# Performance work log

Hardware: AMD Instinct MI355X
Metric: run time of the kernel (lower is better)

## Reference

```python
import jax, jax.numpy as jnp
import numpy as np

B, S, D = 4, 2048, 1024
H = 16
DK = D // H  # 64, dim_k == dim_v
FF = 4096
EPS = 1e-5


def layer_norm(x, g, b):
    mu = jnp.mean(x, axis=-1, keepdims=True)
    var = jnp.mean(jnp.square(x - mu), axis=-1, keepdims=True)
    return (x - mu) * jax.lax.rsqrt(var + EPS) * g + b


def setup_inputs() -> dict:
    key = jax.random.key(0)
    ks = jax.random.split(key, 16)
    s = 0.02
    return {
        "src": jax.random.normal(ks[0], (B, S, D), jnp.float32),
        # per-head Q/K/V projections (stacked over heads)
        "wq": jax.random.normal(ks[1], (H, D, DK), jnp.float32) * s,
        "bq": jnp.zeros((H, DK), jnp.float32),
        "wk": jax.random.normal(ks[2], (H, D, DK), jnp.float32) * s,
        "bk": jnp.zeros((H, DK), jnp.float32),
        "wv": jax.random.normal(ks[3], (H, D, DK), jnp.float32) * s,
        "bv": jnp.zeros((H, DK), jnp.float32),
        # output projection: concat(H*DK) -> D
        "wo": jax.random.normal(ks[4], (H * DK, D), jnp.float32) * s,
        "bo": jnp.zeros((D,), jnp.float32),
        "ln1_g": jnp.ones((D,), jnp.float32),
        "ln1_b": jnp.zeros((D,), jnp.float32),
        # FFN
        "w1": jax.random.normal(ks[5], (D, FF), jnp.float32) * s,
        "b1": jnp.zeros((FF,), jnp.float32),
        "w2": jax.random.normal(ks[6], (FF, D), jnp.float32) * s,
        "b2": jnp.zeros((D,), jnp.float32),
        "ln2_g": jnp.ones((D,), jnp.float32),
        "ln2_b": jnp.zeros((D,), jnp.float32),
    }


def reference(src, wq, bq, wk, bk, wv, bv, wo, bo, ln1_g, ln1_b,
              w1, b1, w2, b2, ln2_g, ln2_b):
    # per-head projections: [B,S,D] x [H,D,K] -> [B,H,S,K]
    q = jnp.einsum('bsd,hdk->bhsk', src, wq) + bq[None, :, None, :]
    k = jnp.einsum('bsd,hdk->bhsk', src, wk) + bk[None, :, None, :]
    v = jnp.einsum('bsd,hdk->bhsk', src, wv) + bv[None, :, None, :]
    scale = 1.0 / jnp.sqrt(jnp.float32(DK))
    scores = jnp.einsum('bhsk,bhtk->bhst', q, k) * scale  # [B,H,S,S]
    attn = jax.nn.softmax(scores, axis=-1)
    o = jnp.einsum('bhst,bhtv->bhsv', attn, v)            # [B,H,S,DK]
    o = o.transpose(0, 2, 1, 3).reshape(B, S, H * DK)      # concat heads
    attn_out = o @ wo + bo
    x = layer_norm(src + attn_out, ln1_g, ln1_b)
    ff = jax.nn.relu(x @ w1 + b1) @ w2 + b2
    return layer_norm(x + ff, ln2_g, ln2_b)
```

## Files before the change

### kernel.cpp

```cpp
#include <hip/hip_runtime.h>

typedef __bf16 bf16;
typedef __bf16 bf16x8 __attribute__((ext_vector_type(8)));
typedef __bf16 bf16x4 __attribute__((ext_vector_type(4)));
typedef float  f32x4  __attribute__((ext_vector_type(4)));
typedef float  f32x16 __attribute__((ext_vector_type(16)));
typedef unsigned int u32;
typedef int i32x2 __attribute__((ext_vector_type(2)));

#define NB 4
#define NS 2048
#define ND 1024
#define NH 16
#define NDK 64
#define NFF 4096
#define NM (NB*NS)

#define QSCALE 0.18033688f

__device__ __forceinline__ void load_lds16(const void* g, void* l) {
  __builtin_amdgcn_global_load_lds(
      (const __attribute__((address_space(1))) void*)g,
      (__attribute__((address_space(3))) void*)l, 16, 0, 0);
}

__device__ __forceinline__ u32 pack2(float a, float b) {
  union { bf16 h[2]; u32 u; } z;
  z.h[0] = (bf16)a; z.h[1] = (bf16)b;
  return z.u;
}

__device__ __forceinline__ i32x2 pswap(u32 a, u32 b) {
#if __has_builtin(__builtin_amdgcn_permlane32_swap)
  return __builtin_amdgcn_permlane32_swap((int)a, (int)b, false, false);
#else
  u32 x = a, y = b;
  asm volatile("v_permlane32_swap_b32 %0, %1" : "+v"(x), "+v"(y));
  i32x2 r; r[0] = (int)x; r[1] = (int)y; return r;
#endif
}

__global__ __launch_bounds__(256)
void cvt_f32_bf16(const float* __restrict__ in, bf16* __restrict__ out, int n) {
  int i = (blockIdx.x * 256 + threadIdx.x) * 4;
  if (i < n) {
    float4 v = *(const float4*)&in[i];
    bf16x4 o;
    o[0] = (bf16)v.x; o[1] = (bf16)v.y; o[2] = (bf16)v.z; o[3] = (bf16)v.w;
    *(bf16x4*)&out[i] = o;
  }
}

__global__ __launch_bounds__(256)
void transpose_cvt(const float* __restrict__ in, bf16* __restrict__ out,
                   int R, int C, size_t in_bs, size_t out_bs) {
  __shared__ float t[32][33];
  int bx = blockIdx.x, by = blockIdx.y, bz = blockIdx.z;
  const float* ip = in + (size_t)bz * in_bs + (size_t)(bx * 32) * C + by * 32;
  bf16* op = out + (size_t)bz * out_bs + (size_t)(by * 32) * R + bx * 32;
  int x = threadIdx.x & 31, y = threadIdx.x >> 5;
#pragma unroll
  for (int yy = 0; yy < 32; yy += 8)
    t[y + yy][x] = ip[(size_t)(y + yy) * C + x];
  __syncthreads();
#pragma unroll
  for (int yy = 0; yy < 32; yy += 8)
    op[(size_t)(y + yy) * R + x] = (bf16)t[x][y + yy];
}

__global__ __launch_bounds__(256)
void transpose_v(const bf16* __restrict__ v, bf16* __restrict__ vT) {
  __shared__ bf16 t[64][72];
  int st = blockIdx.x;
  int bh = blockIdx.y;
  const bf16* ip = v + ((size_t)bh * NS + st * 64) * NDK;
  bf16* op = vT + (size_t)bh * NDK * NS + st * 64;
  int tid = threadIdx.x;
#pragma unroll
  for (int c = tid; c < 512; c += 256) {
    int r = c >> 3, q = c & 7;
    bf16x8 d = *(const bf16x8*)&ip[(size_t)r * NDK + q * 8];
#pragma unroll
    for (int j = 0; j < 8; j++) t[r][q * 8 + j] = d[j];
  }
  __syncthreads();
#pragma unroll
  for (int c = tid; c < 512; c += 256) {
    int dv = c >> 3, sq = c & 7;
    bf16x8 d;
#pragma unroll
    for (int j = 0; j < 8; j++) d[j] = t[sq * 8 + j][dv];
    *(bf16x8*)&op[(size_t)dv * NS + sq * 8] = d;
  }
}

#define BAR()  __builtin_amdgcn_s_barrier()
#define LGKM0() do { asm volatile("s_waitcnt lgkmcnt(0)" ::: "memory"); \
                     __builtin_amdgcn_sched_barrier(0); } while (0)

template<int BN, int EPI>
__global__ __launch_bounds__(512, 2)
void gemm8p(const bf16* __restrict__ A, const bf16* __restrict__ Bt,
            const float* __restrict__ bias0, const float* __restrict__ bias1,
            const float* __restrict__ bias2, void* __restrict__ out0,
            int M, int N, int K) {
  constexpr int NFR = BN / 64;
  __shared__ __align__(16) bf16 lA[2][256 * 64];
  __shared__ __align__(16) bf16 lB[2][BN * 64];

  const int tid = threadIdx.x, lane = tid & 63, w = tid >> 6;
  const int wr = w >> 2, wn = w & 3;
  const int blane = lane & 15, glane = lane >> 4;

  const int nwg = gridDim.x;
  const int cpx = nwg >> 3;
  const int bid = blockIdx.x;
  const int swzb = (bid & 7) * cpx + (bid >> 3);
  const int gridM = M >> 8;
  const int bm = (swzb % gridM) * 256;
  const int bn = (swzb / gridM) * BN;

  f32x4 acc[8][NFR] = {};
  bf16x8 aF[8], bF[2 * NFR];

  auto stageA = [&](int kt, int h, int b) {
#pragma unroll
    for (int j = 0; j < 2; j++) {
      int ch = w * 128 + j * 64 + lane;
      int r = h * 128 + (ch >> 3), s = ch & 7;
      load_lds16(A + (size_t)(bm + r) * K + kt * 64 + ((s ^ (r & 7)) * 8),
                 &lA[b][(h * 1024 + ch) * 8]);
    }
  };
  auto stageB = [&](int kt, int h, int b) {
    if constexpr (BN == 256) {
#pragma unroll
      for (int j = 0; j < 2; j++) {
        int ch = w * 128 + j * 64 + lane;
        int r = h * 128 + (ch >> 3), s = ch & 7;
        load_lds16(Bt + (size_t)(bn + r) * K + kt * 64 + ((s ^ (r & 7)) * 8),
                   &lB[b][(h * 1024 + ch) * 8]);
      }
    } else {
      int ch = w * 64 + lane;
      int r = h * 64 + (ch >> 3), s = ch & 7;
      load_lds16(Bt + (size_t)(bn + r) * K + kt * 64 + ((s ^ (r & 7)) * 8),
                 &lB[b][(h * 512 + ch) * 8]);
    }
  };
  auto vmwait = [&]() {
    if constexpr (BN == 256) asm volatile("s_waitcnt vmcnt(6)" ::: "memory");
    else                     asm volatile("s_waitcnt vmcnt(4)" ::: "memory");
  };
  auto ldA = [&](int mh, int b) {
#pragma unroll
    for (int mf = 0; mf < 4; mf++)
#pragma unroll
      for (int ks = 0; ks < 2; ks++) {
        int r = wr * 128 + mh * 64 + mf * 16 + blane;
        int s = (ks * 4 + glane) ^ (r & 7);
        aF[mf * 2 + ks] = *(const bf16x8*)&lA[b][r * 64 + s * 8];
      }
  };
  auto ldBh = [&](int nh, int b) {
#pragma unroll
    for (int nq = 0; nq < NFR / 2; nq++)
#pragma unroll
      for (int ks = 0; ks < 2; ks++) {
        int nf = nh * (NFR / 2) + nq;
        int r = wn * (NFR * 16) + nf * 16 + blane;
        int s = (ks * 4 + glane) ^ (r & 7);
        bF[nf * 2 + ks] = *(const bf16x8*)&lB[b][r * 64 + s * 8];
      }
  };

#define MMAQ(mh, nh)  do {                                                  \
    __builtin_amdgcn_s_setprio(1);                                          \
    _Pragma("unroll")                                                       \
    for (int mf = 0; mf < 4; mf++)                                          \
      _Pragma("unroll")                                                     \
      for (int nq = 0; nq < NFR / 2; nq++)                                  \
        _Pragma("unroll")                                                   \
        for (int ks = 0; ks < 2; ks++)                                      \
          acc[(mh) * 4 + mf][(nh) * (NFR / 2) + nq] =                       \
            __builtin_amdgcn_mfma_f32_16x16x32_bf16(                        \
              aF[mf * 2 + ks], bF[((nh) * (NFR / 2) + nq) * 2 + ks],        \
              acc[(mh) * 4 + mf][(nh) * (NFR / 2) + nq], 0, 0, 0);          \
    __builtin_amdgcn_s_setprio(0);                                          \
  } while (0)

  stageB(0, 0, 0); stageB(0, 1, 0); stageA(0, 0, 0); stageA(0, 1, 0);
  stageB(1, 0, 1); stageB(1, 1, 1); stageA(1, 0, 1);
  vmwait();
  BAR();

  const int NT = K >> 6;
  for (int u = 0; u < NT; u += 2) {
    const int t2 = (u + 2 < NT) ? u + 2 : u;
    const int t3 = (u + 3 < NT) ? u + 3 : u + 1;
    ldA(0, 0); ldBh(0, 0);
    stageA(u + 1, 1, 1);
    BAR(); LGKM0(); MMAQ(0, 0); BAR();
    ldBh(1, 0);
    stageB(t2, 0, 0);
    BAR(); LGKM0(); MMAQ(0, 1); BAR();
    ldA(1, 0);
    stageB(t2, 1, 0);
    BAR(); LGKM0(); MMAQ(1, 1); BAR();
    stageA(t2, 0, 0);
    BAR(); MMAQ(1, 0); vmwait(); BAR();
    ldA(0, 1); ldBh(0, 1);
    stageA(t2, 1, 0);
    BAR(); LGKM0(); MMAQ(0, 0); BAR();
    ldBh(1, 1);
    stageB(t3, 0, 1);
    BAR(); LGKM0(); MMAQ(0, 1); BAR();
    ldA(1, 1);
    stageB(t3, 1, 1);
    BAR(); LGKM0(); MMAQ(1, 1); BAR();
    stageA(t3, 0, 1);
    BAR(); MMAQ(1, 0); vmwait(); BAR();
  }

#pragma unroll
  for (int am = 0; am < 8; am++) {
#pragma unroll
    for (int nf = 0; nf < NFR; nf++) {
      int col = bn + wn * (NFR * 16) + nf * 16 + blane;
      int rowb = bm + wr * 128 + (am >> 2) * 64 + (am & 3) * 16 + glane * 4;
      if (EPI == 0) {
        int sel = col >> 10;
        int hh = (col & 1023) >> 6;
        int dv = col & 63;
        const float* bp = (sel == 0) ? bias0 : (sel == 1) ? bias1 : bias2;
        float bias = bp[col & 1023];
        float sc = (sel == 0) ? QSCALE : 1.0f;
        bf16* outb = (bf16*)out0 + (size_t)sel * NB * NH * NS * NDK;
#pragma unroll
        for (int i = 0; i < 4; i++) {
          int row = rowb + i;
          int b_ = row >> 11, s_ = row & 2047;
          outb[(((size_t)(b_ * NH + hh) * NS + s_) * NDK) + dv] = (bf16)((acc[am][nf][i] + bias) * sc);
        }
      } else if (EPI == 1) {
        float bias = bias0[col];
#pragma unroll
        for (int i = 0; i < 4; i++) {
          float v = acc[am][nf][i] + bias;
          v = v > 0.f ? v : 0.f;
          ((bf16*)out0)[(size_t)(rowb + i) * N + col] = (bf16)v;
        }
      } else {
        float bias = bias0[col];
#pragma unroll
        for (int i = 0; i < 4; i++)
          ((float*)out0)[(size_t)(rowb + i) * N + col] = acc[am][nf][i] + bias;
      }
    }
  }
#undef MMAQ
}

__global__ __launch_bounds__(256)
void flash_attn6(const bf16* __restrict__ q, const bf16* __restrict__ k,
                 const bf16* __restrict__ vT, bf16* __restrict__ o) {
  __shared__ __align__(16) bf16 lK[2][64 * 64];
  __shared__ __align__(16) bf16 lV[2][64 * 64];
  const int tid = threadIdx.x, lane = tid & 63, w = tid >> 6;
  const int ql = lane & 31, hi = lane >> 5;

  const int id = blockIdx.x;
  const int xcd = id & 7, sseq = id >> 3;
  const int bh = xcd * 8 + (sseq >> 4);
  const int qt = sseq & 15;

  const size_t hb = (size_t)bh * NS * NDK;
  const int qrow = qt * 128 + w * 32 + ql;

  bf16x8 qf[4];
#pragma unroll
  for (int ks = 0; ks < 4; ks++)
    qf[ks] = *(const bf16x8*)&q[hb + (size_t)qrow * NDK + ks * 16 + hi * 8];

  const int r0 = tid >> 3, s0 = ((tid & 7) ^ (r0 & 7)) * 8;
  const int r1 = r0 + 32, s1 = ((tid & 7) ^ (r1 & 7)) * 8;
  const bf16* k0 = k + hb + (size_t)r0 * NDK + s0;
  const bf16* k1 = k + hb + (size_t)r1 * NDK + s1;
  const bf16* v0 = vT + hb + (size_t)r0 * NS + s0;
  const bf16* v1 = vT + hb + (size_t)r1 * NS + s1;

  f32x16 o0 = {}, o1 = {};
  float ls0 = 0.f, ls1 = 0.f, ls2 = 0.f, ls3 = 0.f;

  load_lds16(k0, &lK[0][tid * 8]);
  load_lds16(k1, &lK[0][(tid + 256) * 8]);
  load_lds16(v0, &lV[0][tid * 8]);
  load_lds16(v1, &lV[0][(tid + 256) * 8]);
  __syncthreads();

  const char* lKc = (const char*)&lK[0][0];
  const char* lVc = (const char*)&lV[0][0];
  const int swz = (ql & 7) << 4;

  for (int t = 0; t < NS / 64; t++) {
    const int cur = t & 1;
    if (t < NS / 64 - 1) {
      const size_t ko = (size_t)(t + 1) * 64 * NDK;
      const int vo = (t + 1) * 64;
      load_lds16(k0 + ko, &lK[cur ^ 1][tid * 8]);
      load_lds16(k1 + ko, &lK[cur ^ 1][(tid + 256) * 8]);
      load_lds16(v0 + vo, &lV[cur ^ 1][tid * 8]);
      load_lds16(v1 + vo, &lV[cur ^ 1][(tid + 256) * 8]);
    }
    const char* Kb = lKc + cur * 8192;
    const char* Vb = lVc + cur * 8192;

    f32x16 st0 = {}, st1 = {};
    __builtin_amdgcn_s_setprio(1);
#pragma unroll
    for (int ks = 0; ks < 4; ks++) {
      int byt = (32 * ks + 16 * hi) ^ swz;
      bf16x8 kf0 = *(const bf16x8*)(Kb + ql * 128 + byt);
      bf16x8 kf1 = *(const bf16x8*)(Kb + (32 + ql) * 128 + byt);
      st0 = __builtin_amdgcn_mfma_f32_32x32x16_bf16(kf0, qf[ks], st0, 0, 0, 0);
      st1 = __builtin_amdgcn_mfma_f32_32x32x16_bf16(kf1, qf[ks], st1, 0, 0, 0);
    }
    __builtin_amdgcn_s_setprio(0);

#pragma unroll
    for (int r = 0; r < 16; r += 4) {
      float p00 = exp2f(st0[r]),     p01 = exp2f(st0[r + 1]);
      float p02 = exp2f(st0[r + 2]), p03 = exp2f(st0[r + 3]);
      float p10 = exp2f(st1[r]),     p11 = exp2f(st1[r + 1]);
      float p12 = exp2f(st1[r + 2]), p13 = exp2f(st1[r + 3]);
      st0[r] = p00; st0[r + 1] = p01; st0[r + 2] = p02; st0[r + 3] = p03;
      st1[r] = p10; st1[r + 1] = p11; st1[r + 2] = p12; st1[r + 3] = p13;
      ls0 += p00 + p10; ls1 += p01 + p11;
      ls2 += p02 + p12; ls3 += p03 + p13;
    }

#pragma unroll
    for (int tt = 0; tt < 2; tt++) {
      f32x16 stv = (tt == 0) ? st0 : st1;
      u32 wv[8];
#pragma unroll
      for (int i = 0; i < 8; i++) wv[i] = pack2(stv[2 * i], stv[2 * i + 1]);
#pragma unroll
      for (int kk = 0; kk < 2; kk++) {
        const int base = 4 * kk;
        i32x2 e0 = pswap(wv[base + 0], wv[base + 2]);
        i32x2 e1 = pswap(wv[base + 1], wv[base + 3]);
        union { u32 u[4]; bf16x8 v; } pf;
        pf.u[0] = (u32)e0[0];
        pf.u[1] = (u32)e1[0];
        pf.u[2] = (u32)e0[1];
        pf.u[3] = (u32)e1[1];
        const int ks = 2 * tt + kk;
        int vbyt = (32 * ks + 16 * hi) ^ swz;
        bf16x8 vf0 = *(const bf16x8*)(Vb + ql * 128 + vbyt);
        bf16x8 vf1 = *(const bf16x8*)(Vb + (32 + ql) * 128 + vbyt);
        __builtin_amdgcn_s_setprio(1);
        o0 = __builtin_amdgcn_mfma_f32_32x32x16_bf16(vf0, pf.v, o0, 0, 0, 0);
        o1 = __builtin_amdgcn_mfma_f32_32x32x16_bf16(vf1, pf.v, o1, 0, 0, 0);
        __builtin_amdgcn_s_setprio(0);
      }
    }
    __syncthreads();
  }

  float ls = (ls0 + ls1) + (ls2 + ls3);
  float lR;
  {
    i32x2 sr = pswap((u32)__float_as_int(ls), (u32)__float_as_int(ls));
    float lsp = __int_as_float(hi ? sr[0] : sr[1]);
    float lo_ = hi ? lsp : ls, hi_ = hi ? ls : lsp;
    lR = lo_ + hi_;
  }
  float invl = 1.0f / lR;
  int b_ = bh >> 4, h_ = bh & 15;
  bf16* ob = o + ((size_t)(b_ * NS + qrow) * (NH * NDK)) + h_ * NDK;
#pragma unroll
  for (int rp = 0; rp < 8; rp++) {
    int dv = 8 * (rp >> 1) + 2 * (rp & 1) + 4 * hi;
    *(u32*)&ob[dv]      = pack2(o0[2 * rp] * invl, o0[2 * rp + 1] * invl);
    *(u32*)&ob[dv + 32] = pack2(o1[2 * rp] * invl, o1[2 * rp + 1] * invl);
  }
}

template<int WB>
__global__ __launch_bounds__(256)
void ln_res(const float* __restrict__ a, const float* __restrict__ b,
            const float* __restrict__ g, const float* __restrict__ be,
            float* __restrict__ y, bf16* __restrict__ yb) {
  int row = blockIdx.x;
  int tid = threadIdx.x;
  const float4* a4 = (const float4*)(a + (size_t)row * ND);
  const float4* b4 = (const float4*)(b + (size_t)row * ND);
  float4 av = a4[tid], bv = b4[tid];
  float x0 = av.x + bv.x, x1 = av.y + bv.y, x2 = av.z + bv.z, x3 = av.w + bv.w;
  float s = x0 + x1 + x2 + x3;
  float qq_ = x0 * x0 + x1 * x1 + x2 * x2 + x3 * x3;
#pragma unroll
  for (int d = 1; d < 64; d <<= 1) { s += __shfl_xor(s, d); qq_ += __shfl_xor(qq_, d); }
  __shared__ float ss[4], sq[4];
  int w = tid >> 6, lane = tid & 63;
  if (lane == 0) { ss[w] = s; sq[w] = qq_; }
  __syncthreads();
  s = ss[0] + ss[1] + ss[2] + ss[3];
  qq_ = sq[0] + sq[1] + sq[2] + sq[3];
  float mu = s * (1.0f / ND);
  float var = qq_ * (1.0f / ND) - mu * mu;
  float rs = 1.0f / sqrtf(var + 1e-5f);
  const float4* g4 = (const float4*)g;
  const float4* e4 = (const float4*)be;
  float4 gv = g4[tid], ev = e4[tid];
  float o0 = (x0 - mu) * rs * gv.x + ev.x;
  float o1 = (x1 - mu) * rs * gv.y + ev.y;
  float o2 = (x2 - mu) * rs * gv.z + ev.z;
  float o3 = (x3 - mu) * rs * gv.w + ev.w;
  float4 ov = {o0, o1, o2, o3};
  *(float4*)(y + (size_t)row * ND + tid * 4) = ov;
  if (WB) {
    bf16x4 wv;
    wv[0] = (bf16)o0; wv[1] = (bf16)o1; wv[2] = (bf16)o2; wv[3] = (bf16)o3;
    *(bf16x4*)&yb[(size_t)row * ND + tid * 4] = wv;
  }
}

extern "C" void kernel_launch(void* const* d_in, const int* in_sizes, int n_in,
                              void* d_out, int out_size, void* d_ws, size_t ws_size,
                              hipStream_t stream) {
  const float* src = (const float*)d_in[0];
  const float* wq  = (const float*)d_in[1];
  const float* bq  = (const float*)d_in[2];
  const float* wk  = (const float*)d_in[3];
  const float* bk  = (const float*)d_in[4];
  const float* wv  = (const float*)d_in[5];
  const float* bv  = (const float*)d_in[6];
  const float* wo  = (const float*)d_in[7];
  const float* bo  = (const float*)d_in[8];
  const float* g1  = (const float*)d_in[9];
  const float* be1 = (const float*)d_in[10];
  const float* w1  = (const float*)d_in[11];
  const float* b1  = (const float*)d_in[12];
  const float* w2  = (const float*)d_in[13];
  const float* b2  = (const float*)d_in[14];
  const float* g2  = (const float*)d_in[15];
  const float* be2 = (const float*)d_in[16];

  char* ws = (char*)d_ws;
  bf16*  srcb  = (bf16*)(ws + 0);
  bf16*  wqkvT = (bf16*)(ws + 16777216);
  bf16*  woT   = (bf16*)(ws + 23068672);
  bf16*  w1T   = (bf16*)(ws + 25165824);
  bf16*  w2T   = (bf16*)(ws + 33554432);
  bf16*  qkv   = (bf16*)(ws + 41943040);
  bf16*  vT    = (bf16*)(ws + 92274688);
  bf16*  attno = (bf16*)(ws + 109051904);
  float* tmpf  = (float*)(ws + 125829120);
  float* x     = (float*)(ws + 159383552);
  bf16*  xb    = (bf16*)(ws + 192937984);
  bf16*  hbuf  = qkv;

  const size_t QKVSZ = (size_t)NB * NH * NS * NDK;

  cvt_f32_bf16<<<8192, 256, 0, stream>>>(src, srcb, NM * ND);
  transpose_cvt<<<dim3(32, 2, 16), 256, 0, stream>>>(wq, wqkvT,               1024, 64, 65536, 65536);
  transpose_cvt<<<dim3(32, 2, 16), 256, 0, stream>>>(wk, wqkvT + 1024 * 1024, 1024, 64, 65536, 65536);
  transpose_cvt<<<dim3(32, 2, 16), 256, 0, stream>>>(wv, wqkvT + 2048 * 1024, 1024, 64, 65536, 65536);
  transpose_cvt<<<dim3(32, 32, 1), 256, 0, stream>>>(wo, woT, 1024, 1024, 0, 0);
  transpose_cvt<<<dim3(32, 128, 1), 256, 0, stream>>>(w1, w1T, 1024, 4096, 0, 0);
  transpose_cvt<<<dim3(128, 32, 1), 256, 0, stream>>>(w2, w2T, 4096, 1024, 0, 0);

  gemm8p<256, 0><<<384, 512, 0, stream>>>(srcb, wqkvT, bq, bk, bv, qkv, NM, 3072, 1024);
  transpose_v<<<dim3(32, 64), 256, 0, stream>>>(qkv + 2 * QKVSZ, vT);
  flash_attn6<<<1024, 256, 0, stream>>>(qkv, qkv + QKVSZ, vT, attno);
  gemm8p<128, 2><<<256, 512, 0, stream>>>(attno, woT, bo, nullptr, nullptr, tmpf, NM, 1024, 1024);
  ln_res<1><<<8192, 256, 0, stream>>>(src, tmpf, g1, be1, x, xb);
  gemm8p<256, 1><<<512, 512, 0, stream>>>(xb, w1T, b1, nullptr, nullptr, hbuf, NM, 4096, 1024);
  gemm8p<128, 2><<<256, 512, 0, stream>>>(hbuf, w2T, b2, nullptr, nullptr, tmpf, NM, 1024, 4096);
  ln_res<0><<<8192, 256, 0, stream>>>(x, tmpf, g2, be2, (float*)d_out, nullptr);
}
```

Baseline: 486.6 us.

## Use 512-thread attention blocks with register-staged K/V prefetch

The flash attention kernel now runs 8 waves per block covering 256 query rows, so each K/V tile staged in LDS is shared by twice as many query rows. Each thread loads one 16-byte K and one V chunk per tile. The direct global-to-LDS loads are replaced by register prefetches issued before the compute and written to the other LDS buffer after it, followed by an explicit lgkmcnt wait and s_barrier. This halves K/V global traffic per query and overlaps loads with MFMA work. It costs extra registers, fewer blocks (512) across the CUs, and a barrier shared by more waves.

```diff
diff --git a/kernel.cpp b/kernel.cpp
--- a/kernel.cpp
+++ b/kernel.cpp
@@ -7,6 +7,7 @@
 typedef float  f32x16 __attribute__((ext_vector_type(16)));
 typedef unsigned int u32;
 typedef int i32x2 __attribute__((ext_vector_type(2)));
+typedef int i32x4 __attribute__((ext_vector_type(4)));
 
 #define NB 4
 #define NS 2048
@@ -261,8 +262,8 @@
 #undef MMAQ
 }
 
-__global__ __launch_bounds__(256)
-void flash_attn6(const bf16* __restrict__ q, const bf16* __restrict__ k,
+__global__ __launch_bounds__(512)
+void flash_attn7(const bf16* __restrict__ q, const bf16* __restrict__ k,
                  const bf16* __restrict__ vT, bf16* __restrict__ o) {
   __shared__ __align__(16) bf16 lK[2][64 * 64];
   __shared__ __align__(16) bf16 lV[2][64 * 64];
@@ -271,49 +272,49 @@
 
   const int id = blockIdx.x;
   const int xcd = id & 7, sseq = id >> 3;
-  const int bh = xcd * 8 + (sseq >> 4);
-  const int qt = sseq & 15;
+  const int bh = xcd * 8 + (sseq >> 3);
+  const int qt = sseq & 7;
 
   const size_t hb = (size_t)bh * NS * NDK;
-  const int qrow = qt * 128 + w * 32 + ql;
+  const int qrow = qt * 256 + w * 32 + ql;
 
   bf16x8 qf[4];
 #pragma unroll
   for (int ks = 0; ks < 4; ks++)
     qf[ks] = *(const bf16x8*)&q[hb + (size_t)qrow * NDK + ks * 16 + hi * 8];
 
-  const int r0 = tid >> 3, s0 = ((tid & 7) ^ (r0 & 7)) * 8;
-  const int r1 = r0 + 32, s1 = ((tid & 7) ^ (r1 & 7)) * 8;
-  const bf16* k0 = k + hb + (size_t)r0 * NDK + s0;
-  const bf16* k1 = k + hb + (size_t)r1 * NDK + s1;
-  const bf16* v0 = vT + hb + (size_t)r0 * NS + s0;
-  const bf16* v1 = vT + hb + (size_t)r1 * NS + s1;
+  const int sr = tid >> 3, sc = ((tid & 7) ^ (sr & 7)) * 8;
+  const bf16* ksrc = k  + hb + (size_t)sr * NDK + sc;
+  const bf16* vsrc = vT + hb + (size_t)sr * NS  + sc;
 
   f32x16 o0 = {}, o1 = {};
   float ls0 = 0.f, ls1 = 0.f, ls2 = 0.f, ls3 = 0.f;
-
-  load_lds16(k0, &lK[0][tid * 8]);
-  load_lds16(k1, &lK[0][(tid + 256) * 8]);
-  load_lds16(v0, &lV[0][tid * 8]);
-  load_lds16(v1, &lV[0][(tid + 256) * 8]);
-  __syncthreads();
+  const int swz = (ql & 7) << 4;
+
+  {
+    i32x4 rk = *(const i32x4*)ksrc;
+    i32x4 rv = *(const i32x4*)vsrc;
+    *(i32x4*)&lK[0][tid * 8] = rk;
+    *(i32x4*)&lV[0][tid * 8] = rv;
+  }
+  asm volatile("s_waitcnt lgkmcnt(0)" ::: "memory");
+  __builtin_amdgcn_sched_barrier(0);
+  __builtin_amdgcn_s_barrier();
 
   const char* lKc = (const char*)&lK[0][0];
   const char* lVc = (const char*)&lV[0][0];
-  const int swz = (ql & 7) << 4;
 
   for (int t = 0; t < NS / 64; t++) {
     const int cur = t & 1;
-    if (t < NS / 64 - 1) {
-      const size_t ko = (size_t)(t + 1) * 64 * NDK;
-      const int vo = (t + 1) * 64;
-      load_lds16(k0 + ko, &lK[cur ^ 1][tid * 8]);
-      load_lds16(k1 + ko, &lK[cur ^ 1][(tid + 256) * 8]);
-      load_lds16(v0 + vo, &lV[cur ^ 1][tid * 8]);
-      load_lds16(v1 + vo, &lV[cur ^ 1][(tid + 256) * 8]);
-    }
     const char* Kb = lKc + cur * 8192;
     const char* Vb = lVc + cur * 8192;
+
+    i32x4 nk, nv;
+    const bool pf = (t < NS / 64 - 1);
+    if (pf) {
+      nk = *(const i32x4*)(ksrc + (size_t)(t + 1) * 64 * NDK);
+      nv = *(const i32x4*)(vsrc + (t + 1) * 64);
+    }
 
     f32x16 st0 = {}, st1 = {};
     __builtin_amdgcn_s_setprio(1);
@@ -350,29 +351,36 @@
         const int base = 4 * kk;
         i32x2 e0 = pswap(wv[base + 0], wv[base + 2]);
         i32x2 e1 = pswap(wv[base + 1], wv[base + 3]);
-        union { u32 u[4]; bf16x8 v; } pf;
-        pf.u[0] = (u32)e0[0];
-        pf.u[1] = (u32)e1[0];
-        pf.u[2] = (u32)e0[1];
-        pf.u[3] = (u32)e1[1];
+        union { u32 u[4]; bf16x8 v; } pf_;
+        pf_.u[0] = (u32)e0[0];
+        pf_.u[1] = (u32)e1[0];
+        pf_.u[2] = (u32)e0[1];
+        pf_.u[3] = (u32)e1[1];
         const int ks = 2 * tt + kk;
         int vbyt = (32 * ks + 16 * hi) ^ swz;
         bf16x8 vf0 = *(const bf16x8*)(Vb + ql * 128 + vbyt);
         bf16x8 vf1 = *(const bf16x8*)(Vb + (32 + ql) * 128 + vbyt);
         __builtin_amdgcn_s_setprio(1);
-        o0 = __builtin_amdgcn_mfma_f32_32x32x16_bf16(vf0, pf.v, o0, 0, 0, 0);
-        o1 = __builtin_amdgcn_mfma_f32_32x32x16_bf16(vf1, pf.v, o1, 0, 0, 0);
+        o0 = __builtin_amdgcn_mfma_f32_32x32x16_bf16(vf0, pf_.v, o0, 0, 0, 0);
+        o1 = __builtin_amdgcn_mfma_f32_32x32x16_bf16(vf1, pf_.v, o1, 0, 0, 0);
         __builtin_amdgcn_s_setprio(0);
       }
     }
-    __syncthreads();
+
+    if (pf) {
+      *(i32x4*)&lK[cur ^ 1][tid * 8] = nk;
+      *(i32x4*)&lV[cur ^ 1][tid * 8] = nv;
+    }
+    asm volatile("s_waitcnt lgkmcnt(0)" ::: "memory");
+    __builtin_amdgcn_sched_barrier(0);
+    __builtin_amdgcn_s_barrier();
   }
 
   float ls = (ls0 + ls1) + (ls2 + ls3);
   float lR;
   {
-    i32x2 sr = pswap((u32)__float_as_int(ls), (u32)__float_as_int(ls));
-    float lsp = __int_as_float(hi ? sr[0] : sr[1]);
+    i32x2 sr2 = pswap((u32)__float_as_int(ls), (u32)__float_as_int(ls));
+    float lsp = __int_as_float(hi ? sr2[0] : sr2[1]);
     float lo_ = hi ? lsp : ls, hi_ = hi ? ls : lsp;
     lR = lo_ + hi_;
   }
@@ -474,7 +482,7 @@
 
   gemm8p<256, 0><<<384, 512, 0, stream>>>(srcb, wqkvT, bq, bk, bv, qkv, NM, 3072, 1024);
   transpose_v<<<dim3(32, 64), 256, 0, stream>>>(qkv + 2 * QKVSZ, vT);
-  flash_attn6<<<1024, 256, 0, stream>>>(qkv, qkv + QKVSZ, vT, attno);
+  flash_attn7<<<512, 512, 0, stream>>>(qkv, qkv + QKVSZ, vT, attno);
   gemm8p<128, 2><<<256, 512, 0, stream>>>(attno, woT, bo, nullptr, nullptr, tmpf, NM, 1024, 1024);
   ln_res<1><<<8192, 256, 0, stream>>>(src, tmpf, g1, be1, x, xb);
   gemm8p<256, 1><<<512, 512, 0, stream>>>(xb, w1T, b1, nullptr, nullptr, hbuf, NM, 4096, 1024);
```

Result: faster. 457.5 us (-6.0%).
